# Performance work log

Hardware: AMD Instinct MI355X
Metric: run time of the kernel (lower is better)

Reference implementation:

```python
import jax, jax.numpy as jnp
import numpy as np

N_NODES = 100000
N_EDGES = 1600000
D = 128
NUM_LAYERS = 3
BN_EPS = 1e-5


def setup_inputs() -> dict:
    key = jax.random.key(0)
    k1, k2, k3 = jax.random.split(key, 3)
    x = jax.random.normal(k1, (N_NODES, D), dtype=jnp.float32)
    edge_index = jax.random.randint(k2, (2, N_EDGES), 0, N_NODES, dtype=jnp.int32)
    # xavier-uniform-ish scale for relu gain
    scale = jnp.sqrt(2.0) * jnp.sqrt(6.0 / (D + D))
    Ws = jax.random.uniform(k3, (NUM_LAYERS, D, D), dtype=jnp.float32, minval=-1.0, maxval=1.0) * scale
    gammas = jnp.ones((NUM_LAYERS - 1, D), dtype=jnp.float32)
    betas = jnp.zeros((NUM_LAYERS - 1, D), dtype=jnp.float32)
    return {"x": x, "edge_index": edge_index, "Ws": Ws, "gammas": gammas, "betas": betas}


def gcn_conv(x, W, src, dst, num_nodes):
    # GCNConv(normalize=False, bias=False): linear then scatter-add aggregation
    h = x @ W                               # [N, D]
    msgs = h[src]                           # [E, D] irregular gather
    return jax.ops.segment_sum(msgs, dst, num_segments=num_nodes)  # [N, D] scatter-add


def batch_norm(x, gamma, beta):
    # training-mode BN over node dim, biased variance (torch semantics), deterministic
    mu = jnp.mean(x, axis=0)
    var = jnp.var(x, axis=0)
    return (x - mu) * jax.lax.rsqrt(var + BN_EPS) * gamma + beta


def reference(x, edge_index, Ws, gammas, betas):
    src, dst = edge_index[0], edge_index[1]
    n = x.shape[0]
    for i in range(NUM_LAYERS):
        x = gcn_conv(x, Ws[i], src, dst, n)
        if i != NUM_LAYERS - 1:
            x = batch_norm(x, gammas[i], betas[i])
            x = jax.nn.relu(x)
            # dropout omitted for a deterministic reference (eval-equivalent)
    return jax.nn.log_softmax(x, axis=-1)
```

## Files before the change

kernel.cpp:

```cpp
#include <hip/hip_runtime.h>

#define BN_EPS 1e-5f

typedef __attribute__((ext_vector_type(8))) short bf16x8;
typedef __attribute__((ext_vector_type(4))) float f32x4;

union VU {
    uint4 u;
    bf16x8 b;
};


__global__ __launch_bounds__(256) void hist_k(const int* __restrict__ dst, int E,
                                              int* __restrict__ ghist, int NB) {
    __shared__ int lh[128];
    if (threadIdx.x < 128) lh[threadIdx.x] = 0;
    __syncthreads();
    for (int i = blockIdx.x * 256 + threadIdx.x; i < E; i += gridDim.x * 256)
        atomicAdd(&lh[dst[i] >> 10], 1);
    __syncthreads();
    if (threadIdx.x < 128 && threadIdx.x < NB && lh[threadIdx.x])
        atomicAdd(&ghist[threadIdx.x * 16], lh[threadIdx.x]);
}

__global__ __launch_bounds__(128) void pscan_k(const int* __restrict__ ghist, int NB,
                                               int* __restrict__ sbase, int* __restrict__ csrB,
                                               int* __restrict__ rowptr, int n, int E) {
    __shared__ int pa[128], pc[128];
    int t = threadIdx.x;
    int v = (t < NB) ? ghist[t * 16] : 0;
    int vp = (v + 15) & ~15;
    pa[t] = vp;
    pc[t] = v;
    __syncthreads();
    for (int s = 1; s < 128; s <<= 1) {
        int ta = (t >= s) ? pa[t - s] : 0;
        int tc = (t >= s) ? pc[t - s] : 0;
        __syncthreads();
        pa[t] += ta;
        pc[t] += tc;
        __syncthreads();
    }
    if (t < NB) {
        sbase[t] = pa[t] - vp;
        csrB[t] = pc[t] - v;
        if (t == NB - 1) {
            csrB[NB] = pc[t];
            rowptr[n] = E;
        }
    }
}

#define CHUNK 2048
__global__ __launch_bounds__(256) void bin_k(const int* __restrict__ src, const int* __restrict__ dst, int E,
                                             const int* __restrict__ sbase, int* __restrict__ snext,
                                             int* __restrict__ staged, int NB) {
    __shared__ int hist[128];
    __shared__ int base[128];
    int t = threadIdx.x;
    int c0 = blockIdx.x * CHUNK;
    if (c0 >= E) return;
    if (t < 128) hist[t] = 0;
    __syncthreads();
    int bk[8], pk[8], rk[8];
#pragma unroll
    for (int k = 0; k < 8; ++k) {
        int i = c0 + k * 256 + t;
        bk[k] = -1;
        if (i < E) {
            int d = dst[i];
            int b = d >> 10;
            bk[k] = b;
            pk[k] = src[i] | ((d & 1023) << 17);
            rk[k] = atomicAdd(&hist[b], 1);
        }
    }
    __syncthreads();
    if (t < NB) base[t] = sbase[t] + atomicAdd(&snext[t * 16], hist[t]);
    __syncthreads();
#pragma unroll
    for (int k = 0; k < 8; ++k)
        if (bk[k] >= 0) staged[base[bk[k]] + rk[k]] = pk[k];
}

__global__ __launch_bounds__(1024) void csr_k(const int* __restrict__ staged, const int* __restrict__ ghist,
                                              const int* __restrict__ sbase, const int* __restrict__ csrB,
                                              int* __restrict__ rowptr, int* __restrict__ ssrc, int n) {
    __shared__ int hist[1024], cur[1024];
    int b = blockIdx.x, t = threadIdx.x;
    int nodeBase = b << 10;
    hist[t] = 0;
    __syncthreads();
    int s0 = sbase[b], c = ghist[b * 16];
    for (int j = t; j < c; j += 1024) atomicAdd(&hist[staged[s0 + j] >> 17], 1);
    __syncthreads();
    int v = hist[t];
    for (int s = 1; s < 1024; s <<= 1) {
        int tv = (t >= s) ? hist[t - s] : 0;
        __syncthreads();
        hist[t] += tv;
        __syncthreads();
    }
    int ex = hist[t] - v;
    int cb = csrB[b];
    if (nodeBase + t < n) rowptr[nodeBase + t] = cb + ex;
    cur[t] = ex;
    __syncthreads();
    for (int j = t; j < c; j += 1024) {
        int e = staged[s0 + j];
        int p = atomicAdd(&cur[e >> 17], 1);
        ssrc[cb + p] = e & 131071;
    }
}


static __device__ __forceinline__ unsigned short f2bf(float f) {
    unsigned u = __float_as_uint(f);
    unsigned r = (u + 0x7FFFu + ((u >> 16) & 1u)) >> 16;
    return (unsigned short)r;
}
static __device__ __forceinline__ float bf_lo(unsigned u) { return __uint_as_float(u << 16); }
static __device__ __forceinline__ float bf_hi(unsigned u) { return __uint_as_float(u & 0xFFFF0000u); }


__global__ __launch_bounds__(256) void prepw_k(const float* __restrict__ Ws, uint4* __restrict__ Wp,
                                               int* __restrict__ ghist, int* __restrict__ snext,
                                               float* __restrict__ stats, int* __restrict__ ssrcPad,
                                               unsigned short* __restrict__ h, int NB16, int n, int np) {
    int id = blockIdx.x * 256 + threadIdx.x;
    if (id < NB16) ghist[id] = 0;
    else if (id < 2 * NB16) snext[id - NB16] = 0;
    else if (id < 2 * NB16 + 512) stats[id - 2 * NB16] = 0.f;
    else if (id < 2 * NB16 + 512 + 256) ssrcPad[id - 2 * NB16 - 512] = 0;
    if (id >= 4096 && id < 4096 + 128) {
        int sl = (id - 4096) >> 4, ft = (id - 4096) & 15;
        h[((size_t)sl * np + n) * 16 + ft] = 0;
    }
    if (id >= 3 * 4 * 8 * 64) return;
    int lane = id & 63;
    int nt = (id >> 6) & 7;
    int kt = (id >> 9) & 3;
    int L = id >> 11;
    int quad = lane >> 4, l16 = lane & 15;
    const float* wsrc = Ws + L * 16384 + (kt * 32 + quad * 8) * 128 + nt * 16 + l16;
    unsigned short s[8];
#pragma unroll
    for (int j = 0; j < 8; ++j) s[j] = f2bf(wsrc[j * 128]);
    uint4 pk;
    pk.x = (unsigned)s[0] | ((unsigned)s[1] << 16);
    pk.y = (unsigned)s[2] | ((unsigned)s[3] << 16);
    pk.z = (unsigned)s[4] | ((unsigned)s[5] << 16);
    pk.w = (unsigned)s[6] | ((unsigned)s[7] << 16);
    Wp[id] = pk;
}


template <int MODE>
__global__ __launch_bounds__(256) void mgemm_k(const float* __restrict__ Xf, const unsigned short* __restrict__ Xb,
                                               const uint4* __restrict__ Wp, unsigned short* __restrict__ H,
                                               const float* __restrict__ ss, int n, int np) {
    int lane = threadIdx.x & 63;
    int quad = lane >> 4, l16 = lane & 15;
    int wid = (blockIdx.x * 256 + threadIdx.x) >> 6;
    int nw = (gridDim.x * 256) >> 6;
    int ntiles = (n + 15) >> 4;

    VU b[4][8];
#pragma unroll
    for (int kt = 0; kt < 4; ++kt)
#pragma unroll
        for (int nt = 0; nt < 8; ++nt) b[kt][nt].u = Wp[(kt * 8 + nt) * 64 + lane];

    auto loadA = [&](int tile, VU* a) {
        int row = tile * 16 + l16;
#pragma unroll
        for (int kt = 0; kt < 4; ++kt) {
            float f[8];
            if (MODE == 0) {
                const float* xr = Xf + (size_t)row * 128 + kt * 32 + quad * 8;
                float4 u0 = *(const float4*)(xr);
                float4 u1 = *(const float4*)(xr + 4);
                f[0] = u0.x; f[1] = u0.y; f[2] = u0.z; f[3] = u0.w;
                f[4] = u1.x; f[5] = u1.y; f[6] = u1.z; f[7] = u1.w;
            } else {
                int sl = kt * 2 + (quad >> 1);
                uint4 u = *(const uint4*)(Xb + ((size_t)sl * np + row) * 16 + (quad & 1) * 8);
                f[0] = bf_lo(u.x); f[1] = bf_hi(u.x); f[2] = bf_lo(u.y); f[3] = bf_hi(u.y);
                f[4] = bf_lo(u.z); f[5] = bf_hi(u.z); f[6] = bf_lo(u.w); f[7] = bf_hi(u.w);
                const float4* scp = (const float4*)(ss + kt * 32 + quad * 8);
                const float4* shp = (const float4*)(ss + 128 + kt * 32 + quad * 8);
                float4 c0 = scp[0], c1 = scp[1], d0 = shp[0], d1 = shp[1];
                f[0] = fmaxf(fmaf(f[0], c0.x, d0.x), 0.f);
                f[1] = fmaxf(fmaf(f[1], c0.y, d0.y), 0.f);
                f[2] = fmaxf(fmaf(f[2], c0.z, d0.z), 0.f);
                f[3] = fmaxf(fmaf(f[3], c0.w, d0.w), 0.f);
                f[4] = fmaxf(fmaf(f[4], c1.x, d1.x), 0.f);
                f[5] = fmaxf(fmaf(f[5], c1.y, d1.y), 0.f);
                f[6] = fmaxf(fmaf(f[6], c1.z, d1.z), 0.f);
                f[7] = fmaxf(fmaf(f[7], c1.w, d1.w), 0.f);
            }
            uint4 pk;
            pk.x = (unsigned)f2bf(f[0]) | ((unsigned)f2bf(f[1]) << 16);
            pk.y = (unsigned)f2bf(f[2]) | ((unsigned)f2bf(f[3]) << 16);
            pk.z = (unsigned)f2bf(f[4]) | ((unsigned)f2bf(f[5]) << 16);
            pk.w = (unsigned)f2bf(f[6]) | ((unsigned)f2bf(f[7]) << 16);
            a[kt].u = pk;
        }
    };

    int t = wid;
    VU a[4];
    if (t < ntiles) loadA(t, a);

    while (t < ntiles) {
        int tn = t + nw;
        VU an[4];
        if (tn < ntiles) loadA(tn, an);

        f32x4 acc[8];
#pragma unroll
        for (int nt = 0; nt < 8; ++nt) acc[nt] = (f32x4){0.f, 0.f, 0.f, 0.f};
#pragma unroll
        for (int kt = 0; kt < 4; ++kt)
#pragma unroll
            for (int nt = 0; nt < 8; ++nt)
                acc[nt] = __builtin_amdgcn_mfma_f32_16x16x32_bf16(b[kt][nt].b, a[kt].b, acc[nt], 0, 0, 0);

        int row = t * 16 + l16;
#pragma unroll
        for (int nt = 0; nt < 8; ++nt) {
            uint2 pk;
            pk.x = (unsigned)f2bf(acc[nt][0]) | ((unsigned)f2bf(acc[nt][1]) << 16);
            pk.y = (unsigned)f2bf(acc[nt][2]) | ((unsigned)f2bf(acc[nt][3]) << 16);
            *(uint2*)(H + ((size_t)nt * np + row) * 16 + quad * 4) = pk;
        }

#pragma unroll
        for (int kt = 0; kt < 4; ++kt) a[kt] = an[kt];
        t = tn;
    }
}


template <int MODE>
__global__ __launch_bounds__(256) void aggs_k(const unsigned short* __restrict__ H, const int* __restrict__ rowptr,
                                              const int* __restrict__ ssrc, unsigned* __restrict__ outb,
                                              float* __restrict__ outf, float* __restrict__ stats, int n, int np) {
    __shared__ float sred[4][4][8];
    int slice = blockIdx.x & 7;
    int bg = blockIdx.x >> 3;
    int lane = threadIdx.x & 63;
    int wv = threadIdx.x >> 6;
    int g = lane >> 3;
    int f = lane & 7;
    int wid = bg * 4 + wv;
    int nwave = (gridDim.x >> 3) * 4;
    const unsigned short* hs = H + (size_t)slice * np * 16 + f * 2;
    float s0 = 0, s1 = 0, q0 = 0, q1 = 0;

    for (int base = wid * 8; base < n; base += nwave * 8) {
        int node = base + g;
        bool valid = node < n;
        int cn = valid ? node : (n - 1);
        int beg = rowptr[cn];
        int end = valid ? rowptr[cn + 1] : beg;
        float ax = 0.f, ay = 0.f;

        int md = end - beg;
        md = max(md, __shfl_xor(md, 8));
        md = max(md, __shfl_xor(md, 16));
        md = max(md, __shfl_xor(md, 32));
        int nb = (md + 7) >> 3;

        int idx[8];
#pragma unroll
        for (int k = 0; k < 8; ++k) {
            int j = beg + k;
            idx[k] = (j < end) ? ssrc[j] : n;
        }

        int j0 = beg;
        for (int it = 0; it < nb; ++it) {
            unsigned v[8];
#pragma unroll
            for (int k = 0; k < 8; ++k) v[k] = *(const unsigned*)(hs + (size_t)(unsigned)idx[k] * 16);
            int idn[8];
#pragma unroll
            for (int k = 0; k < 8; ++k) {
                int j = j0 + 8 + k;
                idn[k] = (j < end) ? ssrc[j] : n;
            }
#pragma unroll
            for (int k = 0; k < 8; ++k) {
                ax += bf_lo(v[k]);
                ay += bf_hi(v[k]);
            }
#pragma unroll
            for (int k = 0; k < 8; ++k) idx[k] = idn[k];
            j0 += 8;
        }

        if (MODE == 0) {
            if (valid) outb[((size_t)slice * np + node) * 8 + f] = (unsigned)f2bf(ax) | ((unsigned)f2bf(ay) << 16);
            s0 += ax; q0 += ax * ax;
            s1 += ay; q1 += ay * ay;
        } else {
            if (valid) *(float2*)(outf + (size_t)node * 128 + slice * 16 + f * 2) = make_float2(ax, ay);
        }
    }

    if (MODE == 0) {
        s0 += __shfl_xor(s0, 8); s0 += __shfl_xor(s0, 16); s0 += __shfl_xor(s0, 32);
        s1 += __shfl_xor(s1, 8); s1 += __shfl_xor(s1, 16); s1 += __shfl_xor(s1, 32);
        q0 += __shfl_xor(q0, 8); q0 += __shfl_xor(q0, 16); q0 += __shfl_xor(q0, 32);
        q1 += __shfl_xor(q1, 8); q1 += __shfl_xor(q1, 16); q1 += __shfl_xor(q1, 32);
        if (g == 0) {
            sred[wv][0][f] = s0;
            sred[wv][1][f] = s1;
            sred[wv][2][f] = q0;
            sred[wv][3][f] = q1;
        }
        __syncthreads();
        if (wv == 0 && g == 0) {
            float t0 = (sred[0][0][f] + sred[1][0][f]) + (sred[2][0][f] + sred[3][0][f]);
            float t1 = (sred[0][1][f] + sred[1][1][f]) + (sred[2][1][f] + sred[3][1][f]);
            float t2 = (sred[0][2][f] + sred[1][2][f]) + (sred[2][2][f] + sred[3][2][f]);
            float t3 = (sred[0][3][f] + sred[1][3][f]) + (sred[2][3][f] + sred[3][3][f]);
            atomicAdd(&stats[slice * 16 + 2 * f], t0);
            atomicAdd(&stats[slice * 16 + 2 * f + 1], t1);
            atomicAdd(&stats[128 + slice * 16 + 2 * f], t2);
            atomicAdd(&stats[128 + slice * 16 + 2 * f + 1], t3);
        }
    }
}


__global__ __launch_bounds__(256) void lsm_k(float* __restrict__ out, int n) {
    int lane = threadIdx.x & 63;
    int wid = (blockIdx.x * 256 + threadIdx.x) >> 6;
    int nw = (gridDim.x * 256) >> 6;
    for (int node = wid; node < n; node += nw) {
        float2 v = *(float2*)(out + (size_t)node * 128 + 2 * lane);
        float m = fmaxf(v.x, v.y);
#pragma unroll
        for (int off = 32; off > 0; off >>= 1) m = fmaxf(m, __shfl_xor(m, off));
        float ex = expf(v.x - m) + expf(v.y - m);
#pragma unroll
        for (int off = 32; off > 0; off >>= 1) ex += __shfl_xor(ex, off);
        float lse = m + logf(ex);
        *(float2*)(out + (size_t)node * 128 + 2 * lane) = make_float2(v.x - lse, v.y - lse);
    }
}


__global__ void bnfin_k(const float* __restrict__ stats, const float* __restrict__ gamma,
                        const float* __restrict__ beta, float* __restrict__ ss, int n) {
    int f = threadIdx.x;
    if (f < 128) {
        float mu = stats[f] / n;
        float var = stats[128 + f] / n - mu * mu;
        float rs = rsqrtf(fmaxf(var, 0.f) + BN_EPS);
        float sc = gamma[f] * rs;
        ss[f] = sc;
        ss[128 + f] = beta[f] - mu * sc;
    }
}


extern "C" void kernel_launch(void* const* d_in, const int* in_sizes, int n_in,
                              void* d_out, int out_size, void* d_ws, size_t ws_size,
                              hipStream_t stream) {
    const float* x = (const float*)d_in[0];
    const int* ei = (const int*)d_in[1];
    const float* Ws = (const float*)d_in[2];
    const float* gammas = (const float*)d_in[3];
    const float* betas = (const float*)d_in[4];
    int N = in_sizes[0] / 128;
    int E = in_sizes[1] / 2;
    const int* src = ei;
    const int* dst = ei + E;
    float* out = (float*)d_out;
    int NP = N + 16;

    char* w = (char*)d_ws;
    size_t o = 0;
    auto alloc = [&](size_t bytes) { char* p = w + o; o += (bytes + 511) & ~511ull; return p; };
    unsigned short* h = (unsigned short*)alloc((size_t)NP * 128 * 2);
    unsigned short* h2 = (unsigned short*)alloc((size_t)NP * 128 * 2);
    int* rowptr = (int*)alloc(((size_t)N + 1) * 4);
    int* ssrc = (int*)alloc(((size_t)E + 256) * 4);
    uint4* Wp = (uint4*)alloc(3 * 2048 * 16);
    float* stats = (float*)alloc(512 * 4);
    float* ss = (float*)alloc(512 * 4);

    int NB = (N + 1023) >> 10;
    int* ghist = (int*)alloc((size_t)NB * 16 * 4);
    int* snext = (int*)alloc((size_t)NB * 16 * 4);
    int* sbase = (int*)alloc((size_t)NB * 4);
    int* csrB = (int*)alloc(((size_t)NB + 1) * 4);
    int* staged = (int*)h2;

    prepw_k<<<24, 256, 0, stream>>>(Ws, Wp, ghist, snext, stats, ssrc + E, h, NB * 16, N, NP);
    hist_k<<<256, 256, 0, stream>>>(dst, E, ghist, NB);
    pscan_k<<<1, 128, 0, stream>>>(ghist, NB, sbase, csrB, rowptr, N, E);
    bin_k<<<(E + CHUNK - 1) / CHUNK, 256, 0, stream>>>(src, dst, E, sbase, snext, staged, NB);
    csr_k<<<NB, 1024, 0, stream>>>(staged, ghist, sbase, csrB, rowptr, ssrc, N);

    const int AGG_BLOCKS = 2048;
    const int GEMM_BLOCKS = 512;

    mgemm_k<0><<<GEMM_BLOCKS, 256, 0, stream>>>(x, nullptr, Wp, h, nullptr, N, NP);
    aggs_k<0><<<AGG_BLOCKS, 256, 0, stream>>>(h, rowptr, ssrc, (unsigned*)h2, nullptr, stats, N, NP);
    bnfin_k<<<1, 128, 0, stream>>>(stats, gammas, betas, ss, N);
    mgemm_k<1><<<GEMM_BLOCKS, 256, 0, stream>>>(nullptr, h2, Wp + 2048, h, ss, N, NP);
    aggs_k<0><<<AGG_BLOCKS, 256, 0, stream>>>(h, rowptr, ssrc, (unsigned*)h2, nullptr, stats + 256, N, NP);
    bnfin_k<<<1, 128, 0, stream>>>(stats + 256, gammas + 128, betas + 128, ss + 256, N);
    mgemm_k<1><<<GEMM_BLOCKS, 256, 0, stream>>>(nullptr, h2, Wp + 4096, h, ss + 256, N, NP);
    aggs_k<1><<<AGG_BLOCKS, 256, 0, stream>>>(h, rowptr, ssrc, nullptr, out, nullptr, N, NP);
    lsm_k<<<2048, 256, 0, stream>>>(out, N);
}
```

Baseline: 481.7 us.

## Fuse edge binning and first-layer GEMM into one heterogeneous launch

Merges the edge-binning kernel and the layer-0 GEMM into a single launch, with the first blocks doing binning and the remaining blocks doing the GEMM. The two are independent (binning writes into the h2 staging buffer, the GEMM writes h), so they can overlap on the GPU and one launch plus its tail gap goes away. The cost is a kernel whose register use is set by the heavier GEMM path, which may lower occupancy for the binning blocks, and the shared-memory layout for binning is now carved from a single array.

```diff
diff --git a/kernel.cpp b/kernel.cpp
--- a/kernel.cpp
+++ b/kernel.cpp
@@ -52,13 +52,13 @@
 }
 
 #define CHUNK 2048
-__global__ __launch_bounds__(256) void bin_k(const int* __restrict__ src, const int* __restrict__ dst, int E,
-                                             const int* __restrict__ sbase, int* __restrict__ snext,
-                                             int* __restrict__ staged, int NB) {
-    __shared__ int hist[128];
-    __shared__ int base[128];
+
+static __device__ __forceinline__ void bin_body(const int* __restrict__ src, const int* __restrict__ dst, int E,
+                                                const int* __restrict__ sbase, int* __restrict__ snext,
+                                                int* __restrict__ staged, int NB, int bid,
+                                                int* hist, int* base) {
     int t = threadIdx.x;
-    int c0 = blockIdx.x * CHUNK;
+    int c0 = bid * CHUNK;
     if (c0 >= E) return;
     if (t < 128) hist[t] = 0;
     __syncthreads();
@@ -156,13 +156,11 @@
 
 
 template <int MODE>
-__global__ __launch_bounds__(256) void mgemm_k(const float* __restrict__ Xf, const unsigned short* __restrict__ Xb,
-                                               const uint4* __restrict__ Wp, unsigned short* __restrict__ H,
-                                               const float* __restrict__ ss, int n, int np) {
+static __device__ __forceinline__ void gemm_body(const float* __restrict__ Xf, const unsigned short* __restrict__ Xb,
+                                                 const uint4* __restrict__ Wp, unsigned short* __restrict__ H,
+                                                 const float* __restrict__ ss, int n, int np, int wid, int nw) {
     int lane = threadIdx.x & 63;
     int quad = lane >> 4, l16 = lane & 15;
-    int wid = (blockIdx.x * 256 + threadIdx.x) >> 6;
-    int nw = (gridDim.x * 256) >> 6;
     int ntiles = (n + 15) >> 4;
 
     VU b[4][8];
@@ -241,6 +239,31 @@
     }
 }
 
+template <int MODE>
+__global__ __launch_bounds__(256) void mgemm_k(const float* __restrict__ Xf, const unsigned short* __restrict__ Xb,
+                                               const uint4* __restrict__ Wp, unsigned short* __restrict__ H,
+                                               const float* __restrict__ ss, int n, int np) {
+    int wid = (blockIdx.x * 256 + threadIdx.x) >> 6;
+    int nw = (gridDim.x * 256) >> 6;
+    gemm_body<MODE>(Xf, Xb, Wp, H, ss, n, np, wid, nw);
+}
+
+
+__global__ __launch_bounds__(256) void bing_k(const int* __restrict__ src, const int* __restrict__ dst, int E,
+                                              const int* __restrict__ sbase, int* __restrict__ snext,
+                                              int* __restrict__ staged, int NB, int BINB, int GEMMB,
+                                              const float* __restrict__ x, const uint4* __restrict__ Wp,
+                                              unsigned short* __restrict__ H, int n, int np) {
+    __shared__ int sh[256];
+    if ((int)blockIdx.x < BINB) {
+        bin_body(src, dst, E, sbase, snext, staged, NB, blockIdx.x, sh, sh + 128);
+    } else {
+        int wid = ((blockIdx.x - BINB) * 256 + threadIdx.x) >> 6;
+        int nw = (GEMMB * 256) >> 6;
+        gemm_body<0>(x, nullptr, Wp, H, nullptr, n, np, wid, nw);
+    }
+}
+
 
 template <int MODE>
 __global__ __launch_bounds__(256) void aggs_k(const unsigned short* __restrict__ H, const int* __restrict__ rowptr,
@@ -403,13 +426,15 @@
     prepw_k<<<24, 256, 0, stream>>>(Ws, Wp, ghist, snext, stats, ssrc + E, h, NB * 16, N, NP);
     hist_k<<<256, 256, 0, stream>>>(dst, E, ghist, NB);
     pscan_k<<<1, 128, 0, stream>>>(ghist, NB, sbase, csrB, rowptr, N, E);
-    bin_k<<<(E + CHUNK - 1) / CHUNK, 256, 0, stream>>>(src, dst, E, sbase, snext, staged, NB);
-    csr_k<<<NB, 1024, 0, stream>>>(staged, ghist, sbase, csrB, rowptr, ssrc, N);
 
     const int AGG_BLOCKS = 2048;
     const int GEMM_BLOCKS = 512;
-
-    mgemm_k<0><<<GEMM_BLOCKS, 256, 0, stream>>>(x, nullptr, Wp, h, nullptr, N, NP);
+    int BINB = (E + CHUNK - 1) / CHUNK;
+
+    bing_k<<<BINB + GEMM_BLOCKS, 256, 0, stream>>>(src, dst, E, sbase, snext, staged, NB, BINB, GEMM_BLOCKS,
+                                                   x, Wp, h, N, NP);
+    csr_k<<<NB, 1024, 0, stream>>>(staged, ghist, sbase, csrB, rowptr, ssrc, N);
+
     aggs_k<0><<<AGG_BLOCKS, 256, 0, stream>>>(h, rowptr, ssrc, (unsigned*)h2, nullptr, stats, N, NP);
     bnfin_k<<<1, 128, 0, stream>>>(stats, gammas, betas, ss, N);
     mgemm_k<1><<<GEMM_BLOCKS, 256, 0, stream>>>(nullptr, h2, Wp + 2048, h, ss, N, NP);
```

New measurement: 487.1 us. Within noise of the previous version (+1.1%).
